# Optimization experiments

Measured on AMD Instinct MI355X. Metric: run time of the kernel, lower is better.

The kernel has to match this reference:

```python
import jax, jax.numpy as jnp
import numpy as np

HEADS = 8
DIM_HEAD = 128
LN_EPS = 1e-5


def setup_inputs() -> dict:
    key = jax.random.key(0)
    ks = jax.random.split(key, 4)
    N, M, C, V, T = 64, 2, 64, 15, 256
    dim = C * V              # 960
    inner = HEADS * DIM_HEAD # 1024
    return {
        "x": jax.random.normal(ks[0], (N, M, C, V, T), dtype=jnp.float32),
        "ln_g": jnp.ones((dim,), jnp.float32),
        "ln_b": jnp.zeros((dim,), jnp.float32),
        "w_qkv": jax.random.normal(ks[1], (dim, 3 * inner), dtype=jnp.float32) * (dim ** -0.5),
        "w_out": jax.random.normal(ks[2], (inner, dim), dtype=jnp.float32) * (inner ** -0.5),
        "b_out": jnp.zeros((dim,), jnp.float32),
        "w_lin": jax.random.normal(ks[3], (T, T), dtype=jnp.float32) * (T ** -0.5),
        "b_lin": jnp.zeros((T,), jnp.float32),
    }


def reference(x, ln_g, ln_b, w_qkv, w_out, b_out, w_lin, b_lin):
    N, M, C, V, T = x.shape
    dim = C * V
    # [N, M, C, V, T] -> [N*M, T, C*V]
    xs = jnp.transpose(x, (0, 1, 4, 2, 3)).reshape(N * M, T, dim)

    # PreNorm (LayerNorm over last dim)
    mu = jnp.mean(xs, axis=-1, keepdims=True)
    var = jnp.mean(jnp.square(xs - mu), axis=-1, keepdims=True)
    xn = (xs - mu) * jax.lax.rsqrt(var + LN_EPS) * ln_g + ln_b

    # Attention
    qkv = xn @ w_qkv  # [NM, T, 3*inner]
    q, k, v = jnp.split(qkv, 3, axis=-1)
    def to_heads(t):
        return jnp.transpose(t.reshape(N * M, T, HEADS, DIM_HEAD), (0, 2, 1, 3))
    q, k, v = to_heads(q), to_heads(k), to_heads(v)  # [NM, H, T, D]
    scale = DIM_HEAD ** -0.5
    dots = jnp.einsum('nhid,nhjd->nhij', q, k) * scale
    attn = jax.nn.softmax(dots, axis=-1)
    out = jnp.einsum('nhij,nhjd->nhid', attn, v)
    out = jnp.transpose(out, (0, 2, 1, 3)).reshape(N * M, T, HEADS * DIM_HEAD)
    out = out @ w_out + b_out

    # Residual
    xs = out + xs

    # back to [N, M, C, V, T], then Linear over T + tanh
    x2 = jnp.transpose(xs.reshape(N, M, T, C, V), (0, 1, 3, 4, 2))
    y = jnp.tanh(x2 @ w_lin.T + b_lin)
    return y
```

## Files before the change

kernel.cpp:

```cpp
#include <hip/hip_runtime.h>

typedef unsigned short ushort;
using short8 = __attribute__((ext_vector_type(8))) short;
using f32x4  = __attribute__((ext_vector_type(4))) float;
using i32x4  = __attribute__((ext_vector_type(4))) int;
using us4    = __attribute__((ext_vector_type(4))) ushort;

static __device__ __forceinline__ float bf2f(ushort u) {
  union { unsigned int i; float f; } x; x.i = ((unsigned int)u) << 16; return x.f;
}
static __device__ __forceinline__ ushort f2bf(float f) {
  union { float f; unsigned int i; } x; x.f = f;
  unsigned int u = x.i;
  unsigned int r = u + 0x7fffu + ((u >> 16) & 1u);
  return (ushort)(r >> 16);
}

#define GLOAD16(gp, lp)                                                   \
  __builtin_amdgcn_global_load_lds(                                      \
      (const __attribute__((address_space(1))) void*)(gp),               \
      (__attribute__((address_space(3))) void*)(lp), 16, 0, 0)

__global__ __launch_bounds__(256) void wtrans_kernel(const float* __restrict__ in,
                                                     ushort* __restrict__ out,
                                                     int R, int C) {
  __shared__ float sl[32][33];
  int tx = threadIdx.x & 31, ty = threadIdx.x >> 5;
  int c0 = blockIdx.x * 32, r0 = blockIdx.y * 32;
#pragma unroll
  for (int s = 0; s < 4; s++) {
    int r = r0 + ty + s * 8;
    int c = c0 + tx;
    sl[ty + s * 8][tx] = (c < C) ? in[(size_t)r * C + c] : 0.f;
  }
  __syncthreads();
#pragma unroll
  for (int s = 0; s < 4; s++) {
    int c = c0 + ty + s * 8;
    int r = r0 + tx;
    out[(size_t)c * R + r] = f2bf(sl[tx][ty + s * 8]);
  }
}

__global__ void wsplit_kernel(const float* __restrict__ in, ushort* __restrict__ hi,
                              ushort* __restrict__ lo, int n) {
  int i = blockIdx.x * 256 + threadIdx.x;
  if (i < n) {
    float v = in[i];
    ushort h = f2bf(v);
    hi[i] = h;
    lo[i] = f2bf(v - bf2f(h));
  }
}

__global__ __launch_bounds__(256) void ln_part_kernel(const float* __restrict__ x,
                                                      float* __restrict__ part) {
  int nm = blockIdx.y, ch = blockIdx.x, t = threadIdx.x;
  float s = 0.f, ss = 0.f;
  const float* base = x + ((size_t)nm * 960 + (size_t)ch * 240) * 256 + t;
#pragma unroll 4
  for (int r = 0; r < 240; r++) {
    float v = base[(size_t)r * 256];
    s += v; ss += v * v;
  }
  float2 o; o.x = s; o.y = ss;
  ((float2*)part)[(nm * 4 + ch) * 256 + t] = o;
}

__global__ __launch_bounds__(256) void ln_stat_kernel(const float* __restrict__ part,
                                                      float* __restrict__ stat) {
  int nm = blockIdx.x, t = threadIdx.x;
  float s = 0.f, ss = 0.f;
#pragma unroll
  for (int ch = 0; ch < 4; ch++) {
    float2 p = ((const float2*)part)[(nm * 4 + ch) * 256 + t];
    s += p.x; ss += p.y;
  }
  float mean = s * (1.f / 960.f);
  float var = ss * (1.f / 960.f) - mean * mean;
  float2 o; o.x = mean; o.y = rsqrtf(var + 1e-5f);
  ((float2*)stat)[nm * 256 + t] = o;
}

__global__ __launch_bounds__(256) void ln_apply_kernel(const float* __restrict__ x,
                                                       const float* __restrict__ stat,
                                                       const float* __restrict__ g,
                                                       const float* __restrict__ b,
                                                       ushort* __restrict__ xn) {
  __shared__ float sl[64][65];
  int nm = blockIdx.y;
  int tb = blockIdx.x & 3, cvb = blockIdx.x >> 2;
  int t0 = tb * 64, cv0 = cvb * 64;
  int tx = threadIdx.x & 63, ty = threadIdx.x >> 6;
#pragma unroll
  for (int s = 0; s < 16; s++) {
    int r = ty + s * 4;
    sl[r][tx] = x[((size_t)nm * 960 + cv0 + r) * 256 + t0 + tx];
  }
  __syncthreads();
  float gg = g[cv0 + tx], bb = b[cv0 + tx];
#pragma unroll
  for (int s = 0; s < 16; s++) {
    int tt = ty + s * 4;
    float2 ms = ((const float2*)stat)[nm * 256 + t0 + tt];
    float v = (sl[tx][tt] - ms.x) * ms.y * gg + bb;
    xn[((size_t)nm * 256 + t0 + tt) * 960 + cv0 + tx] = f2bf(v);
  }
}

template <int MODE>
__global__ __launch_bounds__(512, 2) void gemm256(
    const ushort* __restrict__ A, int lda, const ushort* __restrict__ BT, int ldb, int nkt,
    const ushort* __restrict__ Alo, const ushort* __restrict__ Blo,
    ushort* __restrict__ o0, ushort* __restrict__ o1, ushort* __restrict__ o2,
    const float* __restrict__ bias, float* __restrict__ fout) {
  __shared__ char smem[65536];
  int tid = threadIdx.x;
  int l = tid & 63, w = tid >> 6;
  int wr = w >> 2, wc = w & 3;
  int lr = l & 15, lg = l >> 4;
  int cb = blockIdx.x * 256, rb = blockIdx.y * 256;

  int sr = tid >> 2;
  int sl_ = ((tid & 3) ^ ((tid >> 3) & 3)) * 8;
  char* ldsA0 = smem + w * 1024;
  char* ldsB0 = smem + 32768 + w * 1024;

  int swz = (lg ^ ((lr >> 1) & 3)) << 4;
  const char* ArdB = smem + (wr * 128 + lr) * 64 + swz;
  const char* BrdB = smem + 32768 + (wc * 64 + lr) * 64 + swz;

  auto stage = [&](int kt, int buf) {
    const ushort* Ap; const ushort* Bp; int k0;
    if (MODE == 2) {
      int seg = kt >> 3; k0 = (kt & 7) * 32;
      Ap = (seg == 2) ? Alo : A;
      Bp = (seg == 1) ? Blo : BT;
    } else { Ap = A; Bp = BT; k0 = kt * 32; }
    const ushort* ga = Ap + (size_t)(rb + sr) * lda + k0 + sl_;
    const ushort* gb = Bp + (size_t)(cb + sr) * ldb + k0 + sl_;
    GLOAD16(ga,                     ldsA0 + buf * 16384);
    GLOAD16(ga + (size_t)128 * lda, ldsA0 + buf * 16384 + 8192);
    GLOAD16(gb,                     ldsB0 + buf * 16384);
    GLOAD16(gb + (size_t)128 * ldb, ldsB0 + buf * 16384 + 8192);
  };

  f32x4 acc[8][4];
#pragma unroll
  for (int i = 0; i < 8; i++)
#pragma unroll
    for (int j = 0; j < 4; j++) acc[i][j] = (f32x4){0.f, 0.f, 0.f, 0.f};

  stage(0, 0);
  stage(1, 1);
  asm volatile("s_waitcnt vmcnt(4)" ::: "memory");
  __builtin_amdgcn_s_barrier();

  for (int t = 0; t < nkt; t++) {
    int buf = t & 1;
    const char* Ard = ArdB + buf * 16384;
    const char* Brd = BrdB + buf * 16384;
    short8 a[8], b[4];
#pragma unroll
    for (int j = 0; j < 4; j++) b[j] = *(const short8*)(Brd + j * 1024);
#pragma unroll
    for (int i = 0; i < 8; i++) a[i] = *(const short8*)(Ard + i * 1024);
    asm volatile("s_waitcnt lgkmcnt(0)" ::: "memory");
    __builtin_amdgcn_sched_barrier(0);
    __builtin_amdgcn_s_barrier();
    if (t + 2 < nkt) stage(t + 2, buf);
    __builtin_amdgcn_s_setprio(1);
#pragma unroll
    for (int i = 0; i < 8; i++)
#pragma unroll
      for (int j = 0; j < 4; j++)
        acc[i][j] = __builtin_amdgcn_mfma_f32_16x16x32_bf16(a[i], b[j], acc[i][j], 0, 0, 0);
    __builtin_amdgcn_s_setprio(0);
    __builtin_amdgcn_sched_barrier(0);
    if (t + 1 < nkt) {
      if (t + 2 < nkt) asm volatile("s_waitcnt vmcnt(4)" ::: "memory");
      else             asm volatile("s_waitcnt vmcnt(0)" ::: "memory");
      __builtin_amdgcn_s_barrier();
    }
  }

  int row0 = rb + wr * 128, col0 = cb + wc * 64;
  if (MODE == 0) {
    int nm = rb >> 8;
    int which = cb >> 10;
#pragma unroll
    for (int i = 0; i < 8; i++)
#pragma unroll
      for (int j = 0; j < 4; j++) {
        f32x4 v = acc[i][j];
        int col = col0 + j * 16 + lr;
        int cl = col & 1023;
        int h = cl >> 7, d = cl & 127;
        int nmh = nm * 8 + h;
        int t0 = wr * 128 + i * 16 + lg * 4;
        if (which == 2) {
          us4 pk;
          pk.x = f2bf(v[0]); pk.y = f2bf(v[1]); pk.z = f2bf(v[2]); pk.w = f2bf(v[3]);
          *(us4*)&o2[((size_t)nmh * 128 + d) * 256 + t0] = pk;
        } else if (which == 0) {
#pragma unroll
          for (int r = 0; r < 4; r++)
            o0[((size_t)nmh * 256 + t0 + r) * 128 + d] = f2bf(v[r] * 0.08838834764831845f);
        } else {
#pragma unroll
          for (int r = 0; r < 4; r++)
            o1[((size_t)nmh * 256 + t0 + r) * 128 + d] = f2bf(v[r]);
        }
      }
  } else if (MODE == 1) {
#pragma unroll
    for (int i = 0; i < 8; i++)
#pragma unroll
      for (int j = 0; j < 4; j++) {
        f32x4 v = acc[i][j];
        int col = col0 + j * 16 + lr;
        float bb = (col < 960) ? bias[col] : 0.f;
#pragma unroll
        for (int r = 0; r < 4; r++) {
          int row = row0 + i * 16 + lg * 4 + r;
          o0[(size_t)row * 1024 + col] = f2bf(v[r] + bb);
        }
      }
  } else {
#pragma unroll
    for (int i = 0; i < 8; i++)
#pragma unroll
      for (int j = 0; j < 4; j++) {
        f32x4 v = acc[i][j];
        int col = col0 + j * 16 + lr;
        float bb = bias[col];
#pragma unroll
        for (int r = 0; r < 4; r++) {
          int row = row0 + i * 16 + lg * 4 + r;
          fout[(size_t)row * 256 + col] = tanhf(v[r] + bb);
        }
      }
  }
}

__global__ __launch_bounds__(256) void attn_kernel(const ushort* __restrict__ q,
                                                   const ushort* __restrict__ kb,
                                                   const ushort* __restrict__ vT,
                                                   ushort* __restrict__ ao) {
  __shared__ ushort KVs[128 * 72];
  __shared__ ushort Ps[64 * 264];
  int tid = threadIdx.x;
  int l = tid & 63, w = tid >> 6;
  int lr = l & 15, lg = l >> 4;
  int qb = blockIdx.x;
  int nmh = blockIdx.y;

  short8 aq[4];
  {
    const ushort* qp = q + ((size_t)nmh * 256 + qb * 64 + w * 16 + lr) * 128 + lg * 8;
#pragma unroll
    for (int kk = 0; kk < 4; kk++) aq[kk] = *(const short8*)(qp + kk * 32);
  }

  f32x4 s_acc[16];
#pragma unroll
  for (int f = 0; f < 16; f++) s_acc[f] = (f32x4){0.f, 0.f, 0.f, 0.f};

  for (int ct = 0; ct < 4; ct++) {
    __syncthreads();
#pragma unroll
    for (int u = 0; u < 4; u++) {
      int i = tid + u * 256;
      int r = i >> 4, c = i & 15;
      *(i32x4*)&KVs[r * 136 + c * 8] =
          *(const i32x4*)(kb + ((size_t)nmh * 256 + ct * 64 + r) * 128 + c * 8);
    }
    __syncthreads();
#pragma unroll
    for (int j = 0; j < 4; j++) {
      short8 bk[4];
#pragma unroll
      for (int kk = 0; kk < 4; kk++)
        bk[kk] = *(const short8*)&KVs[(j * 16 + lr) * 136 + kk * 32 + lg * 8];
#pragma unroll
      for (int kk = 0; kk < 4; kk++)
        s_acc[ct * 4 + j] =
            __builtin_amdgcn_mfma_f32_16x16x32_bf16(aq[kk], bk[kk], s_acc[ct * 4 + j], 0, 0, 0);
    }
  }

  float m[4] = {-1e30f, -1e30f, -1e30f, -1e30f};
#pragma unroll
  for (int f = 0; f < 16; f++)
#pragma unroll
    for (int r = 0; r < 4; r++) m[r] = fmaxf(m[r], s_acc[f][r]);
#pragma unroll
  for (int dd = 1; dd < 16; dd <<= 1)
#pragma unroll
    for (int r = 0; r < 4; r++) m[r] = fmaxf(m[r], __shfl_xor(m[r], dd, 64));
  float sum[4] = {0.f, 0.f, 0.f, 0.f};
#pragma unroll
  for (int f = 0; f < 16; f++)
#pragma unroll
    for (int r = 0; r < 4; r++) {
      float p = __expf(s_acc[f][r] - m[r]);
      s_acc[f][r] = p;
      sum[r] += p;
    }
#pragma unroll
  for (int dd = 1; dd < 16; dd <<= 1)
#pragma unroll
    for (int r = 0; r < 4; r++) sum[r] += __shfl_xor(sum[r], dd, 64);
  float rs[4];
#pragma unroll
  for (int r = 0; r < 4; r++) rs[r] = 1.f / sum[r];

#pragma unroll
  for (int f = 0; f < 16; f++)
#pragma unroll
    for (int r = 0; r < 4; r++)
      Ps[(w * 16 + lg * 4 + r) * 264 + f * 16 + lr] = f2bf(s_acc[f][r]);

  f32x4 o_acc[8];
#pragma unroll
  for (int j = 0; j < 8; j++) o_acc[j] = (f32x4){0.f, 0.f, 0.f, 0.f};

  for (int ct = 0; ct < 4; ct++) {
    __syncthreads();
#pragma unroll
    for (int u = 0; u < 4; u++) {
      int i = tid + u * 256;
      int r = i >> 3, c = i & 7;
      *(i32x4*)&KVs[r * 72 + c * 8] =
          *(const i32x4*)(vT + ((size_t)nmh * 128 + r) * 256 + ct * 64 + c * 8);
    }
    __syncthreads();
#pragma unroll
    for (int kk = 0; kk < 2; kk++) {
      short8 ap = *(const short8*)&Ps[(w * 16 + lr) * 264 + ct * 64 + kk * 32 + lg * 8];
#pragma unroll
      for (int j = 0; j < 8; j++) {
        short8 bv = *(const short8*)&KVs[(j * 16 + lr) * 72 + kk * 32 + lg * 8];
        o_acc[j] = __builtin_amdgcn_mfma_f32_16x16x32_bf16(ap, bv, o_acc[j], 0, 0, 0);
      }
    }
  }

  int nm = nmh >> 3, h = nmh & 7;
  int trow0 = qb * 64 + w * 16;
#pragma unroll
  for (int j = 0; j < 8; j++)
#pragma unroll
    for (int r = 0; r < 4; r++) {
      int t = trow0 + lg * 4 + r;
      int d = h * 128 + j * 16 + lr;
      ao[((size_t)nm * 256 + t) * 1024 + d] = f2bf(o_acc[j][r] * rs[r]);
    }
}

__global__ __launch_bounds__(256) void x2split_kernel(const float* __restrict__ x,
                                                      const ushort* __restrict__ proj,
                                                      ushort* __restrict__ hi,
                                                      ushort* __restrict__ lo) {
  __shared__ ushort sl[64][65];
  int nm = blockIdx.y;
  int tb = blockIdx.x & 3, cvb = blockIdx.x >> 2;
  int t0 = tb * 64, cv0 = cvb * 64;
  int tx = threadIdx.x & 63, ty = threadIdx.x >> 6;
#pragma unroll
  for (int s = 0; s < 16; s++) {
    int r = ty + s * 4;
    sl[r][tx] = proj[((size_t)nm * 256 + t0 + r) * 1024 + cv0 + tx];
  }
  __syncthreads();
#pragma unroll
  for (int s = 0; s < 16; s++) {
    int cvl = ty + s * 4;
    size_t R = (size_t)nm * 960 + cv0 + cvl;
    float v = x[R * 256 + t0 + tx] + bf2f(sl[tx][cvl]);
    ushort h = f2bf(v);
    hi[R * 256 + t0 + tx] = h;
    lo[R * 256 + t0 + tx] = f2bf(v - bf2f(h));
  }
}

extern "C" void kernel_launch(void* const* d_in, const int* in_sizes, int n_in,
                              void* d_out, int out_size, void* d_ws, size_t ws_size,
                              hipStream_t stream) {
  const float* x = (const float*)d_in[0];
  const float* ln_g = (const float*)d_in[1];
  const float* ln_b = (const float*)d_in[2];
  const float* w_qkv = (const float*)d_in[3];
  const float* w_out = (const float*)d_in[4];
  const float* b_out = (const float*)d_in[5];
  const float* w_lin = (const float*)d_in[6];
  const float* b_lin = (const float*)d_in[7];
  float* out = (float*)d_out;

  char* ws = (char*)d_ws;
  size_t off = 0;
  auto alloc = [&](size_t bytes) -> void* {
    void* p = ws + off;
    off = (off + bytes + 255) & ~(size_t)255;
    return p;
  };

  ushort* wqkvT = (ushort*)alloc((size_t)3072 * 960 * 2);
  ushort* woutT = (ushort*)alloc((size_t)1024 * 1024 * 2);
  ushort* whi   = (ushort*)alloc((size_t)65536 * 2);
  ushort* wlo   = (ushort*)alloc((size_t)65536 * 2);
  float*  part  = (float*)alloc((size_t)128 * 4 * 256 * 2 * 4);
  float*  stat  = (float*)alloc((size_t)32768 * 2 * 4);
  ushort* xn    = (ushort*)alloc((size_t)32768 * 960 * 2);
  ushort* qbuf  = (ushort*)alloc((size_t)1024 * 256 * 128 * 2);
  ushort* kbuf  = (ushort*)alloc((size_t)1024 * 256 * 128 * 2);
  ushort* vTbuf = (ushort*)alloc((size_t)1024 * 256 * 128 * 2);
  ushort* attnout = (ushort*)alloc((size_t)32768 * 1024 * 2);
  ushort* proj = qbuf;
  ushort* x2hi = kbuf;
  ushort* x2lo = vTbuf;

  wtrans_kernel<<<dim3(96, 30), 256, 0, stream>>>(w_qkv, wqkvT, 960, 3072);
  wtrans_kernel<<<dim3(32, 32), 256, 0, stream>>>(w_out, woutT, 1024, 960);
  wsplit_kernel<<<dim3(256), 256, 0, stream>>>(w_lin, whi, wlo, 65536);

  ln_part_kernel<<<dim3(4, 128), 256, 0, stream>>>(x, part);
  ln_stat_kernel<<<dim3(128), 256, 0, stream>>>(part, stat);
  ln_apply_kernel<<<dim3(60, 128), 256, 0, stream>>>(x, stat, ln_g, ln_b, xn);

  gemm256<0><<<dim3(12, 128), 512, 0, stream>>>(xn, 960, wqkvT, 960, 30, nullptr, nullptr,
                                                qbuf, kbuf, vTbuf, nullptr, nullptr);
  attn_kernel<<<dim3(4, 1024), 256, 0, stream>>>(qbuf, kbuf, vTbuf, attnout);
  gemm256<1><<<dim3(4, 128), 512, 0, stream>>>(attnout, 1024, woutT, 1024, 32, nullptr, nullptr,
                                               proj, nullptr, nullptr, b_out, nullptr);
  x2split_kernel<<<dim3(60, 128), 256, 0, stream>>>(x, proj, x2hi, x2lo);
  gemm256<2><<<dim3(1, 480), 512, 0, stream>>>(x2hi, 256, whi, 256, 24, x2lo, wlo,
                                               nullptr, nullptr, nullptr, b_lin, out);
}
```

Measured before the change: 694.4 us.

## Restructure GEMM main loop into 64-wide K steps with staged quarter prefetch

The bf16 GEMM now processes 64 elements of K per iteration, split into four sub-phases that each do 16 MFMAs. Each sub-phase issues one quarter of the next tile's global-to-LDS loads, so memory traffic is interleaved with compute instead of arriving in one burst. LDS use grows from 64KB to 128KB per block with a new swizzle. The aim is fewer loop iterations and better overlap of loads with MFMA work. The cost is more barriers per iteration, and with __launch_bounds__(512,2) the 128KB footprint may prevent two blocks from sharing a CU (160KB LDS on MI355X), which lowers occupancy.

```diff
diff --git a/kernel.cpp b/kernel.cpp
--- a/kernel.cpp
+++ b/kernel.cpp
@@ -114,35 +114,33 @@
     const ushort* __restrict__ Alo, const ushort* __restrict__ Blo,
     ushort* __restrict__ o0, ushort* __restrict__ o1, ushort* __restrict__ o2,
     const float* __restrict__ bias, float* __restrict__ fout) {
-  __shared__ char smem[65536];
+  __shared__ char smem[131072];
   int tid = threadIdx.x;
   int l = tid & 63, w = tid >> 6;
   int wr = w >> 2, wc = w & 3;
   int lr = l & 15, lg = l >> 4;
   int cb = blockIdx.x * 256, rb = blockIdx.y * 256;
 
-  int sr = tid >> 2;
-  int sl_ = ((tid & 3) ^ ((tid >> 3) & 3)) * 8;
-  char* ldsA0 = smem + w * 1024;
-  char* ldsB0 = smem + 32768 + w * 1024;
-
-  int swz = (lg ^ ((lr >> 1) & 3)) << 4;
+  int srow = tid >> 2;
+  int scol = ((tid & 3) ^ ((tid >> 2) & 3)) * 8;
+
+  int swz = (lg ^ (lr & 3)) << 4;
   const char* ArdB = smem + (wr * 128 + lr) * 64 + swz;
-  const char* BrdB = smem + 32768 + (wc * 64 + lr) * 64 + swz;
-
-  auto stage = [&](int kt, int buf) {
-    const ushort* Ap; const ushort* Bp; int k0;
+  const char* BrdB = smem + 65536 + (wc * 64 + lr) * 64 + swz;
+
+  auto stage_half = [&](int kt, int kk, int isB) {
+    const ushort* P; int ld; int k0;
     if (MODE == 2) {
-      int seg = kt >> 3; k0 = (kt & 7) * 32;
-      Ap = (seg == 2) ? Alo : A;
-      Bp = (seg == 1) ? Blo : BT;
-    } else { Ap = A; Bp = BT; k0 = kt * 32; }
-    const ushort* ga = Ap + (size_t)(rb + sr) * lda + k0 + sl_;
-    const ushort* gb = Bp + (size_t)(cb + sr) * ldb + k0 + sl_;
-    GLOAD16(ga,                     ldsA0 + buf * 16384);
-    GLOAD16(ga + (size_t)128 * lda, ldsA0 + buf * 16384 + 8192);
-    GLOAD16(gb,                     ldsB0 + buf * 16384);
-    GLOAD16(gb + (size_t)128 * ldb, ldsB0 + buf * 16384 + 8192);
+      int seg = kt >> 2; k0 = (kt & 3) * 64 + kk * 32;
+      P = isB ? ((seg == 1) ? Blo : BT) : ((seg == 2) ? Alo : A);
+      ld = 256;
+    } else {
+      P = isB ? BT : A; ld = isB ? ldb : lda; k0 = kt * 64 + kk * 32;
+    }
+    const ushort* gp = P + (size_t)((isB ? cb : rb) + srow) * ld + k0 + scol;
+    char* dst = smem + isB * 65536 + (kt & 1) * 32768 + kk * 16384 + tid * 16;
+    GLOAD16(gp, dst);
+    GLOAD16(gp + (size_t)128 * ld, dst + 8192);
   };
 
   f32x4 acc[8][4];
@@ -151,37 +149,75 @@
 #pragma unroll
     for (int j = 0; j < 4; j++) acc[i][j] = (f32x4){0.f, 0.f, 0.f, 0.f};
 
-  stage(0, 0);
-  stage(1, 1);
+  stage_half(0, 0, 0); stage_half(0, 0, 1); stage_half(0, 1, 0); stage_half(0, 1, 1);
   asm volatile("s_waitcnt vmcnt(4)" ::: "memory");
   __builtin_amdgcn_s_barrier();
 
   for (int t = 0; t < nkt; t++) {
-    int buf = t & 1;
-    const char* Ard = ArdB + buf * 16384;
-    const char* Brd = BrdB + buf * 16384;
-    short8 a[8], b[4];
+    const char* Ard = ArdB + (t & 1) * 32768;
+    const char* Brd = BrdB + (t & 1) * 32768;
+    bool st = (t + 1 < nkt);
+    short8 a[4], b[4];
+
 #pragma unroll
     for (int j = 0; j < 4; j++) b[j] = *(const short8*)(Brd + j * 1024);
 #pragma unroll
-    for (int i = 0; i < 8; i++) a[i] = *(const short8*)(Ard + i * 1024);
-    asm volatile("s_waitcnt lgkmcnt(0)" ::: "memory");
-    __builtin_amdgcn_sched_barrier(0);
-    __builtin_amdgcn_s_barrier();
-    if (t + 2 < nkt) stage(t + 2, buf);
+    for (int i = 0; i < 4; i++) a[i] = *(const short8*)(Ard + i * 1024);
+    if (st) stage_half(t + 1, 0, 0);
+    __builtin_amdgcn_s_barrier();
     __builtin_amdgcn_s_setprio(1);
 #pragma unroll
-    for (int i = 0; i < 8; i++)
+    for (int i = 0; i < 4; i++)
 #pragma unroll
       for (int j = 0; j < 4; j++)
         acc[i][j] = __builtin_amdgcn_mfma_f32_16x16x32_bf16(a[i], b[j], acc[i][j], 0, 0, 0);
     __builtin_amdgcn_s_setprio(0);
-    __builtin_amdgcn_sched_barrier(0);
-    if (t + 1 < nkt) {
-      if (t + 2 < nkt) asm volatile("s_waitcnt vmcnt(4)" ::: "memory");
-      else             asm volatile("s_waitcnt vmcnt(0)" ::: "memory");
-      __builtin_amdgcn_s_barrier();
-    }
+    __builtin_amdgcn_s_barrier();
+
+#pragma unroll
+    for (int i = 0; i < 4; i++) a[i] = *(const short8*)(Ard + (4 + i) * 1024);
+    if (st) stage_half(t + 1, 0, 1);
+    __builtin_amdgcn_s_barrier();
+    __builtin_amdgcn_s_setprio(1);
+#pragma unroll
+    for (int i = 0; i < 4; i++)
+#pragma unroll
+      for (int j = 0; j < 4; j++)
+        acc[4 + i][j] = __builtin_amdgcn_mfma_f32_16x16x32_bf16(a[i], b[j], acc[4 + i][j], 0, 0, 0);
+    __builtin_amdgcn_s_setprio(0);
+    if (st) asm volatile("s_waitcnt vmcnt(4)" ::: "memory");
+    else    asm volatile("s_waitcnt vmcnt(0)" ::: "memory");
+    __builtin_amdgcn_s_barrier();
+
+#pragma unroll
+    for (int j = 0; j < 4; j++) b[j] = *(const short8*)(Brd + 16384 + j * 1024);
+#pragma unroll
+    for (int i = 0; i < 4; i++) a[i] = *(const short8*)(Ard + 16384 + i * 1024);
+    if (st) stage_half(t + 1, 1, 0);
+    __builtin_amdgcn_s_barrier();
+    __builtin_amdgcn_s_setprio(1);
+#pragma unroll
+    for (int i = 0; i < 4; i++)
+#pragma unroll
+      for (int j = 0; j < 4; j++)
+        acc[i][j] = __builtin_amdgcn_mfma_f32_16x16x32_bf16(a[i], b[j], acc[i][j], 0, 0, 0);
+    __builtin_amdgcn_s_setprio(0);
+    __builtin_amdgcn_s_barrier();
+
+#pragma unroll
+    for (int i = 0; i < 4; i++) a[i] = *(const short8*)(Ard + 16384 + (4 + i) * 1024);
+    if (st) stage_half(t + 1, 1, 1);
+    __builtin_amdgcn_s_barrier();
+    __builtin_amdgcn_s_setprio(1);
+#pragma unroll
+    for (int i = 0; i < 4; i++)
+#pragma unroll
+      for (int j = 0; j < 4; j++)
+        acc[4 + i][j] = __builtin_amdgcn_mfma_f32_16x16x32_bf16(a[i], b[j], acc[4 + i][j], 0, 0, 0);
+    __builtin_amdgcn_s_setprio(0);
+    if (st) asm volatile("s_waitcnt vmcnt(4)" ::: "memory");
+    else    asm volatile("s_waitcnt vmcnt(0)" ::: "memory");
+    __builtin_amdgcn_s_barrier();
   }
 
   int row0 = rb + wr * 128, col0 = cb + wc * 64;
@@ -428,12 +464,12 @@
   ln_stat_kernel<<<dim3(128), 256, 0, stream>>>(part, stat);
   ln_apply_kernel<<<dim3(60, 128), 256, 0, stream>>>(x, stat, ln_g, ln_b, xn);
 
-  gemm256<0><<<dim3(12, 128), 512, 0, stream>>>(xn, 960, wqkvT, 960, 30, nullptr, nullptr,
+  gemm256<0><<<dim3(12, 128), 512, 0, stream>>>(xn, 960, wqkvT, 960, 15, nullptr, nullptr,
                                                 qbuf, kbuf, vTbuf, nullptr, nullptr);
   attn_kernel<<<dim3(4, 1024), 256, 0, stream>>>(qbuf, kbuf, vTbuf, attnout);
-  gemm256<1><<<dim3(4, 128), 512, 0, stream>>>(attnout, 1024, woutT, 1024, 32, nullptr, nullptr,
+  gemm256<1><<<dim3(4, 128), 512, 0, stream>>>(attnout, 1024, woutT, 1024, 16, nullptr, nullptr,
                                                proj, nullptr, nullptr, b_out, nullptr);
   x2split_kernel<<<dim3(60, 128), 256, 0, stream>>>(x, proj, x2hi, x2lo);
-  gemm256<2><<<dim3(1, 480), 512, 0, stream>>>(x2hi, 256, whi, 256, 24, x2lo, wlo,
+  gemm256<2><<<dim3(1, 480), 512, 0, stream>>>(x2hi, 256, whi, 256, 12, x2lo, wlo,
                                                nullptr, nullptr, nullptr, b_lin, out);
 }
```

Result: no change. 691.4 us (-0.4%).
